# Kernel tuning notes

Hardware: AMD Instinct MI355X
Metric: run time of the kernel (lower is better)

The kernel has to match this reference:

```python
import jax, jax.numpy as jnp
import numpy as np

PCT = 3.0  # normalization_percentile_threshold


def setup_inputs() -> dict:
    key = jax.random.key(0)
    k1, k2 = jax.random.split(key)
    B, C, H, W = 32, 3, 512, 512
    x = jax.random.uniform(k1, (B, C, H, W), dtype=jnp.float32)
    mask = (jax.random.uniform(k2, (B, 1, H, W)) > 0.3).astype(jnp.float32)
    return {"x": x, "mask": mask}


def reference(x, mask):
    B, C, H, W = x.shape
    # --- median padding: fill masked-out region with per-(b,c) median + 0.2 ---
    med = jnp.median(x.reshape(B, C, H * W), axis=-1) + 0.2          # [B, C]
    x = mask * x + (1.0 - mask) * med[:, :, None, None]
    # --- get_hfc: identity in this base-class reference ---
    res = x
    # --- per-(b,c) percentile normalization on 1/256-quantized copy ---
    temp = jnp.trunc(res * 256.0) / 256.0                            # int-quantize (zero-grad, like .int())
    flat = temp.reshape(B, C, H * W)
    lo = jnp.percentile(flat, PCT, axis=-1)[:, :, None, None]        # [B, C, 1, 1]
    hi = jnp.percentile(flat, 100.0 - PCT, axis=-1)[:, :, None, None]
    res = (res - lo) / (hi - lo)
    # --- sub_mask ---
    return res * mask
```

## Files before the change

### kernel.cpp

```cpp
#include <hip/hip_runtime.h>


#define B_       32
#define C_       3
#define BC       (B_ * C_)
#define HW       (512 * 512)
#define BINS     1024
#define QB       256
#define PCT_     3.0
#define CHUNKS1  8
#define CHUNKS3  32

__global__ __launch_bounds__(256) void hist_kernel(
        const float* __restrict__ x, const float* __restrict__ mask,
        unsigned* __restrict__ part) {
    __shared__ unsigned h[BINS];
    const int ch    = blockIdx.x / CHUNKS1;
    const int chunk = blockIdx.x % CHUNKS1;
    const int b     = ch / C_;

    for (int i = threadIdx.x; i < BINS; i += 256) h[i] = 0u;
    __syncthreads();

    const float4* x4 = (const float4*)x    + (size_t)ch * (HW / 4);
    const float4* m4 = (const float4*)mask + (size_t)b  * (HW / 4);
    const int per_chunk = (HW / 4) / CHUNKS1;
    const int base = chunk * per_chunk;

    for (int i = base + threadIdx.x; i < base + per_chunk; i += 256) {
        float4 xv = x4[i];
        float4 mv = m4[i];
        float xs[4] = {xv.x, xv.y, xv.z, xv.w};
        float ms[4] = {mv.x, mv.y, mv.z, mv.w};
#pragma unroll
        for (int j = 0; j < 4; ++j) {
            int mb = (int)(xs[j] * 1024.0f);
            mb = mb < 0 ? 0 : (mb > BINS - 1 ? BINS - 1 : mb);
            unsigned add = 1u + ((ms[j] > 0.5f) ? 0x10000u : 0u);
            atomicAdd(&h[mb], add);
        }
    }
    __syncthreads();

    unsigned* dst = part + (size_t)blockIdx.x * BINS;
    for (int i = threadIdx.x; i < BINS; i += 256) dst[i] = h[i];
}

__global__ __launch_bounds__(256) void stats_kernel(
        const unsigned* __restrict__ part,
        float* __restrict__ loArr, float* __restrict__ scArr) {
    __shared__ unsigned tot[BINS];
    __shared__ unsigned in1024[BINS];
    __shared__ unsigned ps[256];
    __shared__ unsigned s_mbin[2], s_mcum[2], s_mcnt[2];
    __shared__ unsigned s_qtot;
    __shared__ int      s_kb;
    __shared__ int      s_kv[4];
    const int ch = blockIdx.x;
    const int t  = threadIdx.x;

    const unsigned* p = part + (size_t)ch * CHUNKS1 * BINS;
    for (int bin = t; bin < BINS; bin += 256) {
        unsigned tsum = 0, isum = 0;
#pragma unroll
        for (int c = 0; c < CHUNKS1; ++c) {
            unsigned v = p[(size_t)c * BINS + bin];
            tsum += v & 0xFFFFu;
            isum += v >> 16;
        }
        tot[bin]    = tsum;
        in1024[bin] = isum;
    }
    __syncthreads();

    unsigned b0 = tot[4*t], b1 = tot[4*t+1], b2 = tot[4*t+2], b3 = tot[4*t+3];
    unsigned s1 = b0 + b1, s2 = s1 + b2, S = s2 + b3;
    ps[t] = S;
    __syncthreads();
#pragma unroll
    for (int d = 1; d < 256; d <<= 1) {
        unsigned v = (t >= d) ? ps[t - d] : 0u;
        __syncthreads();
        ps[t] += v;
        __syncthreads();
    }
    {
        unsigned excl = ps[t] - S;
        unsigned cp[4] = {excl, excl + b0, excl + s1, excl + s2};
        unsigned ci[4] = {excl + b0, excl + s1, excl + s2, excl + S};
        const unsigned tg0 = HW / 2 - 1, tg1 = HW / 2;
#pragma unroll
        for (int j = 0; j < 4; ++j) {
            if (cp[j] <= tg0 && tg0 < ci[j]) {
                s_mbin[0] = 4*t + j; s_mcum[0] = cp[j]; s_mcnt[0] = ci[j] - cp[j];
            }
            if (cp[j] <= tg1 && tg1 < ci[j]) {
                s_mbin[1] = 4*t + j; s_mcum[1] = cp[j]; s_mcnt[1] = ci[j] - cp[j];
            }
        }
    }
    __syncthreads();

    if (t == 0) {
        const unsigned tgs[2] = {HW / 2 - 1, HW / 2};
        float vals[2];
#pragma unroll
        for (int ti = 0; ti < 2; ++ti) {
            float within = ((float)(tgs[ti] - s_mcum[ti]) + 0.5f) / (float)s_mcnt[ti];
            vals[ti] = ((float)s_mbin[ti] + within) * (1.0f / (float)BINS);
        }
        float med = 0.5f * (vals[0] + vals[1]);
        int kb = (int)((med + 0.2f) * 256.0f);
        s_kb = kb < 0 ? 0 : (kb > QB - 1 ? QB - 1 : kb);
    }
    __syncthreads();

    unsigned v = in1024[4*t] + in1024[4*t+1] + in1024[4*t+2] + in1024[4*t+3];
    ps[t] = v;
    __syncthreads();
#pragma unroll
    for (int d = 1; d < 256; d <<= 1) {
        unsigned u = (t >= d) ? ps[t - d] : 0u;
        __syncthreads();
        ps[t] += u;
        __syncthreads();
    }
    unsigned Q = ps[t];
    if (t == 255) s_qtot = Q;
    __syncthreads();

    {
        const unsigned mo = (unsigned)HW - s_qtot;
        const int kb = s_kb;
        unsigned cp = (Q - v) + ((t >  kb) ? mo : 0u);
        unsigned ci = Q       + ((t >= kb) ? mo : 0u);
        const double rlo = (PCT_ / 100.0) * (double)(HW - 1);
        const double rhi = ((100.0 - PCT_) / 100.0) * (double)(HW - 1);
        const unsigned ilo = (unsigned)rlo, ihi = (unsigned)rhi;
        const unsigned ranks[4] = {ilo, ilo + 1, ihi, ihi + 1};
#pragma unroll
        for (int ri = 0; ri < 4; ++ri)
            if (cp <= ranks[ri] && ranks[ri] < ci) s_kv[ri] = t;
    }
    __syncthreads();

    if (t == 0) {
        const double rlo = (PCT_ / 100.0) * (double)(HW - 1);
        const double rhi = ((100.0 - PCT_) / 100.0) * (double)(HW - 1);
        const unsigned ilo = (unsigned)rlo, ihi = (unsigned)rhi;
        float fl = (float)(rlo - (double)ilo);
        float fh = (float)(rhi - (double)ihi);
        const float inv256 = 1.0f / 256.0f;
        float v0 = (float)s_kv[0] * inv256, v1 = (float)s_kv[1] * inv256;
        float v2 = (float)s_kv[2] * inv256, v3 = (float)s_kv[3] * inv256;
        float lo = v0 + fl * (v1 - v0);
        float hi = v2 + fh * (v3 - v2);
        loArr[ch] = lo;
        scArr[ch] = 1.0f / (hi - lo);
    }
}

__global__ __launch_bounds__(256) void norm_kernel(
        const float* __restrict__ x, const float* __restrict__ mask,
        const float* __restrict__ loArr, const float* __restrict__ scArr,
        float* __restrict__ out) {
    const int ch    = blockIdx.x / CHUNKS3;
    const int chunk = blockIdx.x % CHUNKS3;
    const int b     = ch / C_;
    const float lo = loArr[ch];
    const float sc = scArr[ch];

    const float4* x4 = (const float4*)x    + (size_t)ch * (HW / 4);
    const float4* m4 = (const float4*)mask + (size_t)b  * (HW / 4);
    float4*       o4 = (float4*)out        + (size_t)ch * (HW / 4);
    const int per_chunk = (HW / 4) / CHUNKS3;
    const int base = chunk * per_chunk;

    for (int i = base + threadIdx.x; i < base + per_chunk; i += 256) {
        float4 xv = x4[i];
        float4 mv = m4[i];
        float4 ov;
        ov.x = (mv.x > 0.5f) ? (xv.x - lo) * sc : 0.0f;
        ov.y = (mv.y > 0.5f) ? (xv.y - lo) * sc : 0.0f;
        ov.z = (mv.z > 0.5f) ? (xv.z - lo) * sc : 0.0f;
        ov.w = (mv.w > 0.5f) ? (xv.w - lo) * sc : 0.0f;
        o4[i] = ov;
    }
}

extern "C" void kernel_launch(void* const* d_in, const int* in_sizes, int n_in,
                              void* d_out, int out_size, void* d_ws, size_t ws_size,
                              hipStream_t stream) {
    const float* x    = (const float*)d_in[0];
    const float* mask = (const float*)d_in[1];
    float* out = (float*)d_out;

    unsigned* part  = (unsigned*)d_ws;
    float*    loArr = (float*)(part + BC * CHUNKS1 * BINS);
    float*    scArr = loArr + BC;

    hist_kernel <<<BC * CHUNKS1, 256, 0, stream>>>(x, mask, part);
    stats_kernel<<<BC,           256, 0, stream>>>(part, loArr, scArr);
    norm_kernel <<<BC * CHUNKS3, 256, 0, stream>>>(x, mask, loArr, scArr, out);
}
```

Measured before the change: 65.65 us.

## Fuse histogram and stats kernels via last-block ticket, nontemporal output stores

The separate stats kernel is merged into the histogram kernel. Each block bumps a per-channel ticket counter after writing its partial histogram, and the last block to finish for that channel computes the median and percentiles. This removes one kernel launch and its dependency gap, but adds a hipMemsetAsync to reset the tickets every call. The norm kernel also switches to ext_vector_type loads and nontemporal stores so the output write traffic is streamed rather than cached.

```diff
diff --git a/kernel.cpp b/kernel.cpp
--- a/kernel.cpp
+++ b/kernel.cpp
@@ -11,53 +11,55 @@
 #define CHUNKS1  8
 #define CHUNKS3  32
 
-__global__ __launch_bounds__(256) void hist_kernel(
+typedef float f32x4 __attribute__((ext_vector_type(4)));
+
+__global__ __launch_bounds__(256) void hist_stats_kernel(
         const float* __restrict__ x, const float* __restrict__ mask,
-        unsigned* __restrict__ part) {
+        unsigned* __restrict__ part, unsigned* __restrict__ tickets,
+        float* __restrict__ loArr, float* __restrict__ scArr) {
     __shared__ unsigned h[BINS];
-    const int ch    = blockIdx.x / CHUNKS1;
-    const int chunk = blockIdx.x % CHUNKS1;
-    const int b     = ch / C_;
-
-    for (int i = threadIdx.x; i < BINS; i += 256) h[i] = 0u;
-    __syncthreads();
-
-    const float4* x4 = (const float4*)x    + (size_t)ch * (HW / 4);
-    const float4* m4 = (const float4*)mask + (size_t)b  * (HW / 4);
-    const int per_chunk = (HW / 4) / CHUNKS1;
-    const int base = chunk * per_chunk;
-
-    for (int i = base + threadIdx.x; i < base + per_chunk; i += 256) {
-        float4 xv = x4[i];
-        float4 mv = m4[i];
-        float xs[4] = {xv.x, xv.y, xv.z, xv.w};
-        float ms[4] = {mv.x, mv.y, mv.z, mv.w};
-#pragma unroll
-        for (int j = 0; j < 4; ++j) {
-            int mb = (int)(xs[j] * 1024.0f);
-            mb = mb < 0 ? 0 : (mb > BINS - 1 ? BINS - 1 : mb);
-            unsigned add = 1u + ((ms[j] > 0.5f) ? 0x10000u : 0u);
-            atomicAdd(&h[mb], add);
-        }
-    }
-    __syncthreads();
-
-    unsigned* dst = part + (size_t)blockIdx.x * BINS;
-    for (int i = threadIdx.x; i < BINS; i += 256) dst[i] = h[i];
-}
-
-__global__ __launch_bounds__(256) void stats_kernel(
-        const unsigned* __restrict__ part,
-        float* __restrict__ loArr, float* __restrict__ scArr) {
-    __shared__ unsigned tot[BINS];
     __shared__ unsigned in1024[BINS];
     __shared__ unsigned ps[256];
+    __shared__ unsigned s_rank;
     __shared__ unsigned s_mbin[2], s_mcum[2], s_mcnt[2];
     __shared__ unsigned s_qtot;
     __shared__ int      s_kb;
     __shared__ int      s_kv[4];
-    const int ch = blockIdx.x;
-    const int t  = threadIdx.x;
+
+    const int ch    = blockIdx.x / CHUNKS1;
+    const int chunk = blockIdx.x % CHUNKS1;
+    const int b     = ch / C_;
+    const int t     = threadIdx.x;
+
+    for (int i = t; i < BINS; i += 256) h[i] = 0u;
+    __syncthreads();
+
+    const f32x4* x4 = (const f32x4*)x    + (size_t)ch * (HW / 4);
+    const f32x4* m4 = (const f32x4*)mask + (size_t)b  * (HW / 4);
+    const int per_chunk = (HW / 4) / CHUNKS1;
+    const int base = chunk * per_chunk;
+
+    for (int i = base + t; i < base + per_chunk; i += 256) {
+        f32x4 xv = x4[i];
+        f32x4 mv = m4[i];
+#pragma unroll
+        for (int j = 0; j < 4; ++j) {
+            int mb = (int)(xv[j] * 1024.0f);
+            mb = mb < 0 ? 0 : (mb > BINS - 1 ? BINS - 1 : mb);
+            unsigned add = 1u + ((mv[j] > 0.5f) ? 0x10000u : 0u);
+            atomicAdd(&h[mb], add);
+        }
+    }
+    __syncthreads();
+
+    unsigned* dst = part + (size_t)blockIdx.x * BINS;
+    for (int i = t; i < BINS; i += 256) dst[i] = h[i];
+
+    __threadfence();
+    if (t == 0) s_rank = atomicAdd(&tickets[ch], 1u);
+    __syncthreads();
+    if (s_rank != CHUNKS1 - 1) return;
+    __threadfence();
 
     const unsigned* p = part + (size_t)ch * CHUNKS1 * BINS;
     for (int bin = t; bin < BINS; bin += 256) {
@@ -68,12 +70,12 @@
             tsum += v & 0xFFFFu;
             isum += v >> 16;
         }
-        tot[bin]    = tsum;
+        h[bin]      = tsum;
         in1024[bin] = isum;
     }
     __syncthreads();
 
-    unsigned b0 = tot[4*t], b1 = tot[4*t+1], b2 = tot[4*t+2], b3 = tot[4*t+3];
+    unsigned b0 = h[4*t], b1 = h[4*t+1], b2 = h[4*t+2], b3 = h[4*t+3];
     unsigned s1 = b0 + b1, s2 = s1 + b2, S = s2 + b3;
     ps[t] = S;
     __syncthreads();
@@ -170,21 +172,20 @@
     const float lo = loArr[ch];
     const float sc = scArr[ch];
 
-    const float4* x4 = (const float4*)x    + (size_t)ch * (HW / 4);
-    const float4* m4 = (const float4*)mask + (size_t)b  * (HW / 4);
-    float4*       o4 = (float4*)out        + (size_t)ch * (HW / 4);
+    const f32x4* x4 = (const f32x4*)x    + (size_t)ch * (HW / 4);
+    const f32x4* m4 = (const f32x4*)mask + (size_t)b  * (HW / 4);
+    f32x4*       o4 = (f32x4*)out        + (size_t)ch * (HW / 4);
     const int per_chunk = (HW / 4) / CHUNKS3;
     const int base = chunk * per_chunk;
 
     for (int i = base + threadIdx.x; i < base + per_chunk; i += 256) {
-        float4 xv = x4[i];
-        float4 mv = m4[i];
-        float4 ov;
-        ov.x = (mv.x > 0.5f) ? (xv.x - lo) * sc : 0.0f;
-        ov.y = (mv.y > 0.5f) ? (xv.y - lo) * sc : 0.0f;
-        ov.z = (mv.z > 0.5f) ? (xv.z - lo) * sc : 0.0f;
-        ov.w = (mv.w > 0.5f) ? (xv.w - lo) * sc : 0.0f;
-        o4[i] = ov;
+        f32x4 xv = x4[i];
+        f32x4 mv = m4[i];
+        f32x4 ov;
+#pragma unroll
+        for (int j = 0; j < 4; ++j)
+            ov[j] = (mv[j] > 0.5f) ? (xv[j] - lo) * sc : 0.0f;
+        __builtin_nontemporal_store(ov, &o4[i]);
     }
 }
 
@@ -195,11 +196,14 @@
     const float* mask = (const float*)d_in[1];
     float* out = (float*)d_out;
 
-    unsigned* part  = (unsigned*)d_ws;
-    float*    loArr = (float*)(part + BC * CHUNKS1 * BINS);
-    float*    scArr = loArr + BC;
-
-    hist_kernel <<<BC * CHUNKS1, 256, 0, stream>>>(x, mask, part);
-    stats_kernel<<<BC,           256, 0, stream>>>(part, loArr, scArr);
-    norm_kernel <<<BC * CHUNKS3, 256, 0, stream>>>(x, mask, loArr, scArr, out);
+    unsigned* part    = (unsigned*)d_ws;
+    float*    loArr   = (float*)(part + BC * CHUNKS1 * BINS);
+    float*    scArr   = loArr + BC;
+    unsigned* tickets = (unsigned*)(scArr + BC);
+
+    hipMemsetAsync(tickets, 0, BC * sizeof(unsigned), stream);
+
+    hist_stats_kernel<<<BC * CHUNKS1, 256, 0, stream>>>(x, mask, part, tickets,
+                                                        loArr, scArr);
+    norm_kernel      <<<BC * CHUNKS3, 256, 0, stream>>>(x, mask, loArr, scArr, out);
 }
```

Measured after the change: 153.1 us. +133.2%, slower.
